# Kernel tuning notes

Hardware: AMD Instinct MI355X
Metric: run time of the kernel (lower is better)

The kernel has to match this reference:

```python
import jax, jax.numpy as jnp
import numpy as np

# Config (matches init_kwargs)
D_MODEL = 1024
D_MLP = 4096
N_EXPERTS = 8
TOP_K = 2  # experts_per_token
BATCH = 1
POS = 2048


def setup_inputs() -> dict:
    key = jax.random.key(0)
    k0, k1, k2, k3, k4 = jax.random.split(key, 5)
    s = 0.02  # typical init scale
    x = jax.random.normal(k0, (BATCH, POS, D_MODEL), jnp.float32)
    W_gate = jax.random.normal(k1, (D_MODEL, N_EXPERTS), jnp.float32) * s  # router
    We_gate = jax.random.normal(k2, (N_EXPERTS, D_MODEL, D_MLP), jnp.float32) * s
    We_in = jax.random.normal(k3, (N_EXPERTS, D_MODEL, D_MLP), jnp.float32) * s
    We_out = jax.random.normal(k4, (N_EXPERTS, D_MLP, D_MODEL), jnp.float32) * s
    return {"x": x, "W_gate": W_gate, "We_gate": We_gate, "We_in": We_in, "We_out": We_out}


def reference(x, W_gate, We_gate, We_in, We_out):
    B, P, D = x.shape
    T = B * P
    E = W_gate.shape[1]
    h = x.reshape(T, D)  # [T, D]

    # Router: logits -> fp32 softmax -> top-k -> renormalize (as in torch code)
    logits = h @ W_gate  # [T, E]
    probs = jax.nn.softmax(logits.astype(jnp.float32), axis=-1)
    topw, topi = jax.lax.top_k(probs, TOP_K)  # [T, K]
    topw = topw / jnp.sum(topw, axis=-1, keepdims=True)
    topw = topw.astype(x.dtype)

    # Per-token combine weight for each expert (0 if not routed). [T, E]
    w_full = jnp.zeros((T, E), x.dtype).at[jnp.arange(T)[:, None], topi].add(topw)

    # Gated-MLP per expert; scan over the small fixed expert axis to avoid
    # materializing [E, T, D_MLP] hidden states at once.
    def per_expert(acc, params):
        Wg, Wi, Wo, we = params  # Wg/Wi: [D, D_MLP], Wo: [D_MLP, D], we: [T]
        hid = jax.nn.silu(h @ Wg) * (h @ Wi)  # [T, D_MLP]
        return acc + (hid @ Wo) * we[:, None], None

    res, _ = jax.lax.scan(
        per_expert,
        jnp.zeros((T, D), x.dtype),
        (We_gate, We_in, We_out, w_full.T),
    )
    return res.reshape(B, P, D)
```

## Files before the change

### kernel.cpp

```cpp
#include <hip/hip_runtime.h>
#include <hip/hip_bf16.h>

#define T_TOK 2048
#define DMODEL 1024
#define DMLP 4096
#define NEXP 8

typedef __bf16 bf16x8 __attribute__((ext_vector_type(8)));
typedef float f32x4 __attribute__((ext_vector_type(4)));

__device__ __forceinline__ unsigned short f2bf(float f) {
  return __builtin_bit_cast(unsigned short, (__bf16)f);
}

__global__ __launch_bounds__(64) void router_k(
    const float* __restrict__ x, const float* __restrict__ wg,
    int* __restrict__ topi, float* __restrict__ topw) {
  int t = blockIdx.x;
  int lane = threadIdx.x;
  const float* hx = x + (size_t)t * DMODEL;
  float acc[NEXP];
#pragma unroll
  for (int e = 0; e < NEXP; ++e) acc[e] = 0.f;
  for (int i = lane; i < DMODEL; i += 64) {
    float xi = hx[i];
    const float* w = wg + (size_t)i * NEXP;
#pragma unroll
    for (int e = 0; e < NEXP; ++e) acc[e] += xi * w[e];
  }
#pragma unroll
  for (int off = 32; off > 0; off >>= 1) {
#pragma unroll
    for (int e = 0; e < NEXP; ++e) acc[e] += __shfl_down(acc[e], off);
  }
  if (lane == 0) {
    float m = acc[0];
#pragma unroll
    for (int e = 1; e < NEXP; ++e) m = fmaxf(m, acc[e]);
    float p[NEXP], s = 0.f;
#pragma unroll
    for (int e = 0; e < NEXP; ++e) { p[e] = expf(acc[e] - m); s += p[e]; }
    float inv = 1.f / s;
#pragma unroll
    for (int e = 0; e < NEXP; ++e) p[e] *= inv;
    int i1 = 0;
#pragma unroll
    for (int e = 1; e < NEXP; ++e) if (p[e] > p[i1]) i1 = e;
    int i2 = (i1 == 0) ? 1 : 0;
#pragma unroll
    for (int e = 0; e < NEXP; ++e) if (e != i1 && p[e] > p[i2]) i2 = e;
    float w1 = p[i1], w2 = p[i2];
    float rs = 1.f / (w1 + w2);
    topi[2 * t] = i1;
    topi[2 * t + 1] = i2;
    topw[2 * t] = w1 * rs;
    topw[2 * t + 1] = w2 * rs;
  }
}

__global__ __launch_bounds__(512) void compact_k(
    const int* __restrict__ topi, const float* __restrict__ topw,
    int* __restrict__ offsets, int* __restrict__ perm,
    float* __restrict__ wrow) {
  int tid = threadIdx.x;
  int e = tid >> 6, lane = tid & 63;
  __shared__ int scnt[NEXP];
  __shared__ int soff[NEXP + 1];
  int c = 0;
  for (int j = lane; j < 2 * T_TOK; j += 64) {
    unsigned long long m = __ballot(topi[j] == e);
    c += __popcll(m);
  }
  if (lane == 0) scnt[e] = c;
  __syncthreads();
  if (tid == 0) {
    int s = 0;
    for (int k = 0; k < NEXP; ++k) { soff[k] = s; s += scnt[k]; }
    soff[NEXP] = s;
    for (int k = 0; k <= NEXP; ++k) offsets[k] = soff[k];
  }
  __syncthreads();
  int base = soff[e];
  for (int j = lane; j < 2 * T_TOK; j += 64) {
    bool f = (topi[j] == e);
    unsigned long long m = __ballot(f);
    if (f) {
      int p = base + __popcll(m & ((1ULL << lane) - 1ULL));
      perm[p] = j >> 1;
      wrow[p] = topw[j];
    }
    base += __popcll(m);
  }
}

#define BPITCH 40

__global__ __launch_bounds__(256) void hid_k(
    const float* __restrict__ x, const float* __restrict__ weg,
    const float* __restrict__ wei, const int* __restrict__ offsets,
    const int* __restrict__ perm, const float* __restrict__ wrow,
    unsigned short* __restrict__ hid) {
  int e = blockIdx.z;
  int off = offsets[e], end = offsets[e + 1];
  int cnt = end - off;
  int m0 = blockIdx.y * 128;
  if (m0 >= cnt) return;
  int nb = blockIdx.x * 64;
  const float* wg = weg + (size_t)e * DMODEL * DMLP;
  const float* wi = wei + (size_t)e * DMODEL * DMLP;

  __shared__ unsigned short As[128 * BPITCH];
  __shared__ unsigned short Bg[64 * BPITCH];
  __shared__ unsigned short Bi[64 * BPITCH];

  int tid = threadIdx.x;
  int lane = tid & 63, wid = tid >> 6;
  int wm = (wid & 1) * 64, wn = (wid >> 1) * 32;
  int lr = lane & 15, q = lane >> 4;

  f32x4 accg[4][2], acci[4][2];
  f32x4 z = {0.f, 0.f, 0.f, 0.f};
#pragma unroll
  for (int i = 0; i < 4; ++i)
#pragma unroll
    for (int j = 0; j < 2; ++j) { accg[i][j] = z; acci[i][j] = z; }

  const float* aptr[4];
  int adst[4];
#pragma unroll
  for (int it = 0; it < 4; ++it) {
    int task = tid + it * 256;
    int r = task >> 3, kc = (task & 7) * 4;
    int pl = m0 + r;
    int src = perm[off + ((pl < cnt) ? pl : 0)];
    aptr[it] = x + (size_t)src * DMODEL + kc;
    adst[it] = r * BPITCH + kc;
  }
  int tn = (tid & 15) * 4, tk = (tid >> 4) * 2;

  for (int k0 = 0; k0 < DMODEL; k0 += 32) {
#pragma unroll
    for (int it = 0; it < 4; ++it) {
      float4 v = *(const float4*)(aptr[it] + k0);
      ushort4 u;
      u.x = f2bf(v.x); u.y = f2bf(v.y); u.z = f2bf(v.z); u.w = f2bf(v.w);
      *(ushort4*)(&As[adst[it]]) = u;
    }
    {
      const float* pg = wg + (size_t)(k0 + tk) * DMLP + nb + tn;
      float4 g0 = *(const float4*)(pg);
      float4 g1 = *(const float4*)(pg + DMLP);
      const float* pi = wi + (size_t)(k0 + tk) * DMLP + nb + tn;
      float4 i0 = *(const float4*)(pi);
      float4 i1 = *(const float4*)(pi + DMLP);
      const float* c0 = (const float*)&g0;
      const float* c1 = (const float*)&g1;
      const float* d0 = (const float*)&i0;
      const float* d1 = (const float*)&i1;
#pragma unroll
      for (int cix = 0; cix < 4; ++cix) {
        ushort2 vg; vg.x = f2bf(c0[cix]); vg.y = f2bf(c1[cix]);
        *(ushort2*)(&Bg[(tn + cix) * BPITCH + tk]) = vg;
        ushort2 vi; vi.x = f2bf(d0[cix]); vi.y = f2bf(d1[cix]);
        *(ushort2*)(&Bi[(tn + cix) * BPITCH + tk]) = vi;
      }
    }
    __syncthreads();
    bf16x8 af[4], bgf[2], bif[2];
#pragma unroll
    for (int i = 0; i < 4; ++i)
      af[i] = *(const bf16x8*)(&As[(wm + i * 16 + lr) * BPITCH + q * 8]);
#pragma unroll
    for (int j = 0; j < 2; ++j) {
      bgf[j] = *(const bf16x8*)(&Bg[(wn + j * 16 + lr) * BPITCH + q * 8]);
      bif[j] = *(const bf16x8*)(&Bi[(wn + j * 16 + lr) * BPITCH + q * 8]);
    }
#pragma unroll
    for (int i = 0; i < 4; ++i)
#pragma unroll
      for (int j = 0; j < 2; ++j) {
        accg[i][j] = __builtin_amdgcn_mfma_f32_16x16x32_bf16(af[i], bgf[j], accg[i][j], 0, 0, 0);
        acci[i][j] = __builtin_amdgcn_mfma_f32_16x16x32_bf16(af[i], bif[j], acci[i][j], 0, 0, 0);
      }
    __syncthreads();
  }
#pragma unroll
  for (int i = 0; i < 4; ++i)
#pragma unroll
    for (int j = 0; j < 2; ++j)
#pragma unroll
      for (int r = 0; r < 4; ++r) {
        int row = wm + i * 16 + q * 4 + r;
        int pl = m0 + row;
        if (pl < cnt) {
          int pos = off + pl;
          float g = accg[i][j][r], vv = acci[i][j][r];
          float hv = (g / (1.f + expf(-g))) * vv * wrow[pos];
          hid[(size_t)pos * DMLP + nb + wn + j * 16 + lr] = f2bf(hv);
        }
      }
}

__global__ __launch_bounds__(256) void out_k(
    const unsigned short* __restrict__ hid, const float* __restrict__ weo,
    const int* __restrict__ offsets, const int* __restrict__ perm,
    float* __restrict__ out) {
  int e = blockIdx.z;
  int off = offsets[e], end = offsets[e + 1];
  int cnt = end - off;
  int m0 = blockIdx.y * 128;
  if (m0 >= cnt) return;
  int nb = blockIdx.x * 64;
  const float* wo = weo + (size_t)e * DMLP * DMODEL;

  __shared__ unsigned short As[128 * BPITCH];
  __shared__ unsigned short Bs[64 * BPITCH];

  int tid = threadIdx.x;
  int lane = tid & 63, wid = tid >> 6;
  int wm = (wid & 1) * 64, wn = (wid >> 1) * 32;
  int lr = lane & 15, q = lane >> 4;

  f32x4 acc[4][2];
  f32x4 z = {0.f, 0.f, 0.f, 0.f};
#pragma unroll
  for (int i = 0; i < 4; ++i)
#pragma unroll
    for (int j = 0; j < 2; ++j) acc[i][j] = z;

  const unsigned short* aptr[2];
  int adst[2];
#pragma unroll
  for (int it = 0; it < 2; ++it) {
    int task = tid + it * 256;
    int r = task >> 2, kg = (task & 3) * 8;
    int pl = m0 + r;
    int src = off + ((pl < cnt) ? pl : 0);
    aptr[it] = hid + (size_t)src * DMLP + kg;
    adst[it] = r * BPITCH + kg;
  }
  int tn = (tid & 15) * 4, tk = (tid >> 4) * 2;

  for (int k0 = 0; k0 < DMLP; k0 += 32) {
#pragma unroll
    for (int it = 0; it < 2; ++it) {
      uint4 v = *(const uint4*)(aptr[it] + k0);
      *(uint4*)(&As[adst[it]]) = v;
    }
    {
      const float* pb = wo + (size_t)(k0 + tk) * DMODEL + nb + tn;
      float4 b0 = *(const float4*)(pb);
      float4 b1 = *(const float4*)(pb + DMODEL);
      const float* c0 = (const float*)&b0;
      const float* c1 = (const float*)&b1;
#pragma unroll
      for (int cix = 0; cix < 4; ++cix) {
        ushort2 vb; vb.x = f2bf(c0[cix]); vb.y = f2bf(c1[cix]);
        *(ushort2*)(&Bs[(tn + cix) * BPITCH + tk]) = vb;
      }
    }
    __syncthreads();
    bf16x8 af[4], bf[2];
#pragma unroll
    for (int i = 0; i < 4; ++i)
      af[i] = *(const bf16x8*)(&As[(wm + i * 16 + lr) * BPITCH + q * 8]);
#pragma unroll
    for (int j = 0; j < 2; ++j)
      bf[j] = *(const bf16x8*)(&Bs[(wn + j * 16 + lr) * BPITCH + q * 8]);
#pragma unroll
    for (int i = 0; i < 4; ++i)
#pragma unroll
      for (int j = 0; j < 2; ++j)
        acc[i][j] = __builtin_amdgcn_mfma_f32_16x16x32_bf16(af[i], bf[j], acc[i][j], 0, 0, 0);
    __syncthreads();
  }
#pragma unroll
  for (int i = 0; i < 4; ++i)
#pragma unroll
    for (int j = 0; j < 2; ++j)
#pragma unroll
      for (int r = 0; r < 4; ++r) {
        int row = wm + i * 16 + q * 4 + r;
        int pl = m0 + row;
        if (pl < cnt) {
          int tok = perm[off + pl];
          atomicAdd(&out[(size_t)tok * DMODEL + nb + wn + j * 16 + lr],
                    acc[i][j][r]);
        }
      }
}

extern "C" void kernel_launch(void* const* d_in, const int* in_sizes, int n_in,
                              void* d_out, int out_size, void* d_ws,
                              size_t ws_size, hipStream_t stream) {
  const float* x = (const float*)d_in[0];
  const float* wgate = (const float*)d_in[1];
  const float* weg = (const float*)d_in[2];
  const float* wei = (const float*)d_in[3];
  const float* weo = (const float*)d_in[4];
  float* out = (float*)d_out;

  char* ws = (char*)d_ws;
  int* topi = (int*)(ws + 0);
  float* topw = (float*)(ws + (16 << 10));
  int* offsets = (int*)(ws + (32 << 10));
  int* perm = (int*)(ws + (33 << 10));
  float* wrow = (float*)(ws + (49 << 10));
  unsigned short* hid = (unsigned short*)(ws + (65 << 10));

  hipMemsetAsync(d_out, 0, (size_t)out_size * sizeof(float), stream);
  router_k<<<dim3(T_TOK), dim3(64), 0, stream>>>(x, wgate, topi, topw);
  compact_k<<<dim3(1), dim3(512), 0, stream>>>(topi, topw, offsets, perm, wrow);
  hid_k<<<dim3(DMLP / 64, T_TOK / 128, NEXP), dim3(256), 0, stream>>>(
      x, weg, wei, offsets, perm, wrow, hid);
  out_k<<<dim3(DMODEL / 64, T_TOK / 128, NEXP), dim3(256), 0, stream>>>(
      hid, weo, offsets, perm, out);
}
```

Before: 679.3 us.

## Pre-convert weights to transposed bf16 and use direct-to-LDS loads in expert GEMMs

Adds kernels that convert x to bf16 and transpose the expert weights into K-contiguous bf16 copies each call. New GEMM kernels use global_load_lds 16-byte loads straight into shared memory, and the gate and in products run in a single fused tile. The output GEMM writes per-slot rows to a temp buffer and a combine kernel sums each token's two expert rows, replacing atomics and the output memset. This path only runs when the workspace holds at least 245 MB. The conversion passes add roughly 400 MB of extra traffic per call, which may eat into the GEMM savings.

```diff
diff --git a/kernel.cpp b/kernel.cpp
--- a/kernel.cpp
+++ b/kernel.cpp
@@ -11,6 +11,13 @@
 
 __device__ __forceinline__ unsigned short f2bf(float f) {
   return __builtin_bit_cast(unsigned short, (__bf16)f);
+}
+
+__device__ __forceinline__ void gload16(const unsigned short* g,
+                                        unsigned short* l) {
+  __builtin_amdgcn_global_load_lds(
+      (const __attribute__((address_space(1))) unsigned int*)g,
+      (__attribute__((address_space(3))) unsigned int*)l, 16, 0, 0);
 }
 
 __global__ __launch_bounds__(64) void router_k(
@@ -61,7 +68,7 @@
 __global__ __launch_bounds__(512) void compact_k(
     const int* __restrict__ topi, const float* __restrict__ topw,
     int* __restrict__ offsets, int* __restrict__ perm,
-    float* __restrict__ wrow) {
+    float* __restrict__ wrow, int* __restrict__ inv) {
   int tid = threadIdx.x;
   int e = tid >> 6, lane = tid & 63;
   __shared__ int scnt[NEXP];
@@ -88,9 +95,252 @@
       int p = base + __popcll(m & ((1ULL << lane) - 1ULL));
       perm[p] = j >> 1;
       wrow[p] = topw[j];
+      inv[j] = p;
     }
     base += __popcll(m);
   }
+}
+
+
+__global__ __launch_bounds__(256) void xcvt_k(const float* __restrict__ x,
+                                              unsigned short* __restrict__ xb) {
+  int i = blockIdx.x * 256 + threadIdx.x;
+  float4 v = ((const float4*)x)[i];
+  ushort4 u;
+  u.x = f2bf(v.x); u.y = f2bf(v.y); u.z = f2bf(v.z); u.w = f2bf(v.w);
+  ((ushort4*)xb)[i] = u;
+}
+
+#define TP 72
+
+__global__ __launch_bounds__(256) void tgi_k(
+    const float* __restrict__ weg, const float* __restrict__ wei,
+    unsigned short* __restrict__ wgt, unsigned short* __restrict__ wit) {
+  int z = blockIdx.z; int e = z >> 1; int mat = z & 1;
+  const float* src = (mat ? wei : weg) + (size_t)e * DMODEL * DMLP;
+  unsigned short* dst = (mat ? wit : wgt) + (size_t)e * DMLP * DMODEL;
+  int k0 = blockIdx.y * 64, c0 = blockIdx.x * 64;
+  __shared__ unsigned short tl[64 * TP];
+  int tid = threadIdx.x;
+#pragma unroll
+  for (int i = 0; i < 4; ++i) {
+    int task = tid + i * 256;
+    int r = task >> 4, c4 = (task & 15) * 4;
+    float4 v = *(const float4*)(src + (size_t)(k0 + r) * DMLP + c0 + c4);
+    tl[(c4 + 0) * TP + r] = f2bf(v.x);
+    tl[(c4 + 1) * TP + r] = f2bf(v.y);
+    tl[(c4 + 2) * TP + r] = f2bf(v.z);
+    tl[(c4 + 3) * TP + r] = f2bf(v.w);
+  }
+  __syncthreads();
+#pragma unroll
+  for (int i = 0; i < 2; ++i) {
+    int task = tid + i * 256;
+    int rr = task >> 3, cc = (task & 7) * 8;
+    uint4 v = *(const uint4*)(&tl[rr * TP + cc]);
+    *(uint4*)(dst + (size_t)(c0 + rr) * DMODEL + k0 + cc) = v;
+  }
+}
+
+__global__ __launch_bounds__(256) void tout_k(
+    const float* __restrict__ weo, unsigned short* __restrict__ wot) {
+  int e = blockIdx.z;
+  const float* src = weo + (size_t)e * DMLP * DMODEL;
+  unsigned short* dst = wot + (size_t)e * DMODEL * DMLP;
+  int k0 = blockIdx.y * 64, c0 = blockIdx.x * 64;
+  __shared__ unsigned short tl[64 * TP];
+  int tid = threadIdx.x;
+#pragma unroll
+  for (int i = 0; i < 4; ++i) {
+    int task = tid + i * 256;
+    int r = task >> 4, c4 = (task & 15) * 4;
+    float4 v = *(const float4*)(src + (size_t)(k0 + r) * DMODEL + c0 + c4);
+    tl[(c4 + 0) * TP + r] = f2bf(v.x);
+    tl[(c4 + 1) * TP + r] = f2bf(v.y);
+    tl[(c4 + 2) * TP + r] = f2bf(v.z);
+    tl[(c4 + 3) * TP + r] = f2bf(v.w);
+  }
+  __syncthreads();
+#pragma unroll
+  for (int i = 0; i < 2; ++i) {
+    int task = tid + i * 256;
+    int rr = task >> 3, cc = (task & 7) * 8;
+    uint4 v = *(const uint4*)(&tl[rr * TP + cc]);
+    *(uint4*)(dst + (size_t)(c0 + rr) * DMLP + k0 + cc) = v;
+  }
+}
+
+__global__ __launch_bounds__(256) void hid2_k(
+    const unsigned short* __restrict__ xb, const unsigned short* __restrict__ wgt,
+    const unsigned short* __restrict__ wit, const int* __restrict__ offsets,
+    const int* __restrict__ perm, const float* __restrict__ wrow,
+    unsigned short* __restrict__ hid) {
+  int e = blockIdx.z;
+  int off = offsets[e], end = offsets[e + 1];
+  int cnt = end - off;
+  int m0 = blockIdx.y * 128;
+  if (m0 >= cnt) return;
+  int nb = blockIdx.x * 64;
+
+  __shared__ unsigned short As[128 * 32];
+  __shared__ unsigned short Bs[128 * 32];
+
+  int tid = threadIdx.x;
+  int lane = tid & 63, wid = tid >> 6;
+  int wm = (wid & 1) * 64, wn = (wid >> 1) * 64;
+  int lr = lane & 15, q = lane >> 4;
+
+  f32x4 acc[4][4];
+  f32x4 z = {0.f, 0.f, 0.f, 0.f};
+#pragma unroll
+  for (int i = 0; i < 4; ++i)
+#pragma unroll
+    for (int j = 0; j < 4; ++j) acc[i][j] = z;
+
+  const unsigned short* aptr[2];
+  const unsigned short* bptr[2];
+#pragma unroll
+  for (int it = 0; it < 2; ++it) {
+    int task = tid + it * 256;
+    int r = task >> 2, ch = task & 3;
+    int pl = m0 + r;
+    int src = perm[off + ((pl < cnt) ? pl : 0)];
+    aptr[it] = xb + (size_t)src * DMODEL + ch * 8;
+    int arr = (r >> 5) & 1;
+    int col = nb + (r & 31) + ((r >> 6) << 5);
+    const unsigned short* w =
+        (arr ? wit : wgt) + (size_t)e * DMLP * DMODEL;
+    bptr[it] = w + (size_t)col * DMODEL + ch * 8;
+  }
+
+  for (int k0 = 0; k0 < DMODEL; k0 += 32) {
+#pragma unroll
+    for (int it = 0; it < 2; ++it) {
+      gload16(aptr[it] + k0, &As[(tid + it * 256) * 8]);
+      gload16(bptr[it] + k0, &Bs[(tid + it * 256) * 8]);
+    }
+    __syncthreads();
+    bf16x8 af[4], bfr[4];
+#pragma unroll
+    for (int i = 0; i < 4; ++i)
+      af[i] = *(const bf16x8*)(&As[(wm + i * 16 + lr) * 32 + q * 8]);
+#pragma unroll
+    for (int j = 0; j < 4; ++j)
+      bfr[j] = *(const bf16x8*)(&Bs[(wn + j * 16 + lr) * 32 + q * 8]);
+#pragma unroll
+    for (int i = 0; i < 4; ++i)
+#pragma unroll
+      for (int j = 0; j < 4; ++j)
+        acc[i][j] = __builtin_amdgcn_mfma_f32_16x16x32_bf16(af[i], bfr[j],
+                                                            acc[i][j], 0, 0, 0);
+    __syncthreads();
+  }
+
+  int colbase = nb + (wn ? 32 : 0);
+#pragma unroll
+  for (int i = 0; i < 4; ++i) {
+#pragma unroll
+    for (int jp = 0; jp < 2; ++jp) {
+#pragma unroll
+      for (int r = 0; r < 4; ++r) {
+        int row = wm + i * 16 + q * 4 + r;
+        int pl = m0 + row;
+        if (pl < cnt) {
+          int pos = off + pl;
+          float g = acc[i][jp][r], vv = acc[i][jp + 2][r];
+          float hv = (g / (1.f + expf(-g))) * vv * wrow[pos];
+          hid[(size_t)pos * DMLP + colbase + jp * 16 + lr] = f2bf(hv);
+        }
+      }
+    }
+  }
+}
+
+__global__ __launch_bounds__(256) void out2_k(
+    const unsigned short* __restrict__ hid, const unsigned short* __restrict__ wot,
+    const int* __restrict__ offsets, float* __restrict__ tmp) {
+  int e = blockIdx.z;
+  int off = offsets[e], end = offsets[e + 1];
+  int cnt = end - off;
+  int m0 = blockIdx.y * 128;
+  if (m0 >= cnt) return;
+  int n0 = blockIdx.x * 128;
+
+  __shared__ unsigned short As[128 * 32];
+  __shared__ unsigned short Bs[128 * 32];
+
+  int tid = threadIdx.x;
+  int lane = tid & 63, wid = tid >> 6;
+  int wm = (wid & 1) * 64, wn = (wid >> 1) * 64;
+  int lr = lane & 15, q = lane >> 4;
+
+  f32x4 acc[4][4];
+  f32x4 z = {0.f, 0.f, 0.f, 0.f};
+#pragma unroll
+  for (int i = 0; i < 4; ++i)
+#pragma unroll
+    for (int j = 0; j < 4; ++j) acc[i][j] = z;
+
+  const unsigned short* aptr[2];
+  const unsigned short* bptr[2];
+#pragma unroll
+  for (int it = 0; it < 2; ++it) {
+    int task = tid + it * 256;
+    int r = task >> 2, ch = task & 3;
+    int pl = m0 + r;
+    aptr[it] = hid + (size_t)(off + ((pl < cnt) ? pl : 0)) * DMLP + ch * 8;
+    bptr[it] = wot + (size_t)e * DMODEL * DMLP + (size_t)(n0 + r) * DMLP + ch * 8;
+  }
+
+  for (int k0 = 0; k0 < DMLP; k0 += 32) {
+#pragma unroll
+    for (int it = 0; it < 2; ++it) {
+      gload16(aptr[it] + k0, &As[(tid + it * 256) * 8]);
+      gload16(bptr[it] + k0, &Bs[(tid + it * 256) * 8]);
+    }
+    __syncthreads();
+    bf16x8 af[4], bfr[4];
+#pragma unroll
+    for (int i = 0; i < 4; ++i)
+      af[i] = *(const bf16x8*)(&As[(wm + i * 16 + lr) * 32 + q * 8]);
+#pragma unroll
+    for (int j = 0; j < 4; ++j)
+      bfr[j] = *(const bf16x8*)(&Bs[(wn + j * 16 + lr) * 32 + q * 8]);
+#pragma unroll
+    for (int i = 0; i < 4; ++i)
+#pragma unroll
+      for (int j = 0; j < 4; ++j)
+        acc[i][j] = __builtin_amdgcn_mfma_f32_16x16x32_bf16(af[i], bfr[j],
+                                                            acc[i][j], 0, 0, 0);
+    __syncthreads();
+  }
+
+#pragma unroll
+  for (int i = 0; i < 4; ++i)
+#pragma unroll
+    for (int j = 0; j < 4; ++j)
+#pragma unroll
+      for (int r = 0; r < 4; ++r) {
+        int row = wm + i * 16 + q * 4 + r;
+        int pl = m0 + row;
+        if (pl < cnt) {
+          tmp[(size_t)(off + pl) * DMODEL + n0 + wn + j * 16 + lr] =
+              acc[i][j][r];
+        }
+      }
+}
+
+__global__ __launch_bounds__(256) void comb_k(const float* __restrict__ tmp,
+                                              const int* __restrict__ inv,
+                                              float* __restrict__ out) {
+  int t = blockIdx.x, c = threadIdx.x;
+  int i0 = inv[2 * t], i1 = inv[2 * t + 1];
+  const float4* t4 = (const float4*)tmp;
+  float4 a = t4[(size_t)i0 * 256 + c];
+  float4 b = t4[(size_t)i1 * 256 + c];
+  float4 o;
+  o.x = a.x + b.x; o.y = a.y + b.y; o.z = a.z + b.z; o.w = a.w + b.w;
+  ((float4*)out)[(size_t)t * 256 + c] = o;
 }
 
 #define BPITCH 40
@@ -301,18 +551,40 @@
   float* out = (float*)d_out;
 
   char* ws = (char*)d_ws;
-  int* topi = (int*)(ws + 0);
-  float* topw = (float*)(ws + (16 << 10));
-  int* offsets = (int*)(ws + (32 << 10));
-  int* perm = (int*)(ws + (33 << 10));
-  float* wrow = (float*)(ws + (49 << 10));
-  unsigned short* hid = (unsigned short*)(ws + (65 << 10));
-
-  hipMemsetAsync(d_out, 0, (size_t)out_size * sizeof(float), stream);
+  const size_t KB = 1024, MB = 1048576;
+  int* topi = (int*)(ws + 0 * KB);
+  float* topw = (float*)(ws + 16 * KB);
+  int* offsets = (int*)(ws + 32 * KB);
+  int* perm = (int*)(ws + 33 * KB);
+  float* wrow = (float*)(ws + 49 * KB);
+  int* inv = (int*)(ws + 65 * KB);
+
   router_k<<<dim3(T_TOK), dim3(64), 0, stream>>>(x, wgate, topi, topw);
-  compact_k<<<dim3(1), dim3(512), 0, stream>>>(topi, topw, offsets, perm, wrow);
-  hid_k<<<dim3(DMLP / 64, T_TOK / 128, NEXP), dim3(256), 0, stream>>>(
-      x, weg, wei, offsets, perm, wrow, hid);
-  out_k<<<dim3(DMODEL / 64, T_TOK / 128, NEXP), dim3(256), 0, stream>>>(
-      hid, weo, offsets, perm, out);
-}
+  compact_k<<<dim3(1), dim3(512), 0, stream>>>(topi, topw, offsets, perm, wrow, inv);
+
+  if (ws_size >= (size_t)245 * MB) {
+    unsigned short* xb = (unsigned short*)(ws + 1 * MB);
+    unsigned short* hid = (unsigned short*)(ws + 5 * MB);
+    float* tmp = (float*)(ws + 37 * MB);
+    unsigned short* wgt = (unsigned short*)(ws + 53 * MB);
+    unsigned short* wit = (unsigned short*)(ws + 117 * MB);
+    unsigned short* wot = (unsigned short*)(ws + 181 * MB);
+
+    xcvt_k<<<dim3(T_TOK * DMODEL / 1024), dim3(256), 0, stream>>>(x, xb);
+    tgi_k<<<dim3(DMLP / 64, DMODEL / 64, NEXP * 2), dim3(256), 0, stream>>>(
+        weg, wei, wgt, wit);
+    tout_k<<<dim3(DMODEL / 64, DMLP / 64, NEXP), dim3(256), 0, stream>>>(weo, wot);
+    hid2_k<<<dim3(DMLP / 64, T_TOK / 128, NEXP), dim3(256), 0, stream>>>(
+        xb, wgt, wit, offsets, perm, wrow, hid);
+    out2_k<<<dim3(DMODEL / 128, T_TOK / 128, NEXP), dim3(256), 0, stream>>>(
+        hid, wot, offsets, tmp);
+    comb_k<<<dim3(T_TOK), dim3(256), 0, stream>>>(tmp, inv, out);
+  } else {
+    unsigned short* hid = (unsigned short*)(ws + 96 * KB);
+    hipMemsetAsync(d_out, 0, (size_t)out_size * sizeof(float), stream);
+    hid_k<<<dim3(DMLP / 64, T_TOK / 128, NEXP), dim3(256), 0, stream>>>(
+        x, weg, wei, offsets, perm, wrow, hid);
+    out_k<<<dim3(DMODEL / 64, T_TOK / 128, NEXP), dim3(256), 0, stream>>>(
+        hid, weo, offsets, perm, out);
+  }
+}
```

After: 677.0 us. About the same (-0.3%).
